# Kernel optimization log

Hardware: AMD Instinct MI355X
Metric: run time of the kernel (lower is better)

The kernel has to match this reference:

```python
import jax, jax.numpy as jnp
import numpy as np

B, S, E, H = 8, 1024, 1024, 16
D = E // H            # head_dim = 64
L = 1024              # pos_max_len; rpe table rows = 2*L+1
SCALE = D ** 0.5


def setup_inputs() -> dict:
    key = jax.random.key(0)
    ks = jax.random.split(key, 7)
    x = jax.random.normal(ks[0], (B, S, E), dtype=jnp.float32)
    mask = jnp.tril(jnp.ones((S, S), dtype=bool))[None, None]  # causal [1,1,S,S]
    w = 1.0 / np.sqrt(E)
    Wq = jax.random.normal(ks[1], (E, E), dtype=jnp.float32) * w
    Wk = jax.random.normal(ks[2], (E, E), dtype=jnp.float32) * w
    Wv = jax.random.normal(ks[3], (E, E), dtype=jnp.float32) * w
    Wo = jax.random.normal(ks[4], (E, E), dtype=jnp.float32) * w
    pek_table = jax.random.normal(ks[5], (2 * L + 1, D), dtype=jnp.float32) / D ** 0.5
    pev_table = jax.random.normal(ks[6], (2 * L + 1, D), dtype=jnp.float32) / D ** 0.5
    return {"x": x, "mask": mask, "Wq": Wq, "Wk": Wk, "Wv": Wv, "Wo": Wo,
            "pek_table": pek_table, "pev_table": pev_table}


def reference(x, mask, Wq, Wk, Wv, Wo, pek_table, pev_table):
    # QKV projections (torch Linear: y = x @ W.T), reshaped to [B,H,S,D]
    q = (x @ Wq.T).reshape(B, S, H, D).transpose(0, 2, 1, 3)
    k = (x @ Wk.T).reshape(B, S, H, D).transpose(0, 2, 1, 3)
    v = (x @ Wv.T).reshape(B, S, H, D).transpose(0, 2, 1, 3)

    scores = jnp.einsum('bhsd,bhtd->bhst', q, k) / SCALE  # [B,H,S,S]

    # relative-position embeddings: rel[i,j] selects embedding for offset j-i
    pos = jnp.arange(S)
    rel = jnp.clip(pos[None, :] - pos[:, None] + L, 0, 2 * L)  # [S,S]
    pek = pek_table[rel]  # [S,S,D]
    pev = pev_table[rel]  # [S,S,D]

    # RPE score term, replicating torch view/transpose semantics exactly:
    # Q2: [B,S,H,D] -> [S,B,H,D] -> [S, B*H, D]
    q2 = (x @ Wq.T).reshape(B, S, H, D).transpose(1, 0, 2, 3).reshape(S, B * H, D)
    s2 = jnp.einsum('snd,std->snt', q2, pek)               # [S, B*H, S]
    s2 = s2.reshape(S, H, B, S).transpose(2, 1, 0, 3)      # torch .view(S,H,B,S).transpose(0,2)
    scores = scores + s2 / SCALE

    scores = jnp.where(mask, scores, -jnp.inf)
    attn = jax.nn.softmax(scores, axis=-1)                  # [B,H,S,S]

    out = jnp.einsum('bhst,bhtd->bhsd', attn, v)            # [B,H,S,D]

    # RPE value term: attn.transpose(0,2) -> [S,H,B,S] -> [S, H*B, S]
    a2 = attn.transpose(2, 1, 0, 3).reshape(S, H * B, S)
    o2 = jnp.einsum('snt,std->snd', a2, pev)                # [S, H*B, D]
    o2 = o2.reshape(S, H, B, D).transpose(2, 1, 0, 3)       # [B,H,S,D]
    out = out + o2

    out = out.transpose(0, 2, 1, 3).reshape(B, S, E) @ Wo.T
    return out
```

## Files before the change

kernel.cpp:

```cpp
#include <hip/hip_runtime.h>
#include <math.h>

#define NB 8
#define NS 1024
#define NE 1024
#define NH 16
#define ND 64
#define NL 1024

typedef __attribute__((ext_vector_type(8))) short short8;
typedef __attribute__((ext_vector_type(4))) float f32x4;
typedef __attribute__((ext_vector_type(16))) float f32x16;

__device__ __forceinline__ ushort f2bf(float f) {
    union { __bf16 h; ushort u; } v;
    v.h = (__bf16)f;
    return v.u;
}
__device__ __forceinline__ float bf2f(ushort u) {
    union { unsigned u; float f; } v; v.u = ((unsigned)u) << 16;
    return v.f;
}

__device__ __forceinline__ void stage16(const ushort* gsrc, ushort* lbase) {
    __builtin_amdgcn_global_load_lds((const __attribute__((address_space(1))) void*)gsrc,
                                     (__attribute__((address_space(3))) void*)lbase,
                                     16, 0, 0);
}

__global__ __launch_bounds__(256)
void cast_f2b4(const float* __restrict__ in, ushort* __restrict__ out, int n4) {
    int i = blockIdx.x * 256 + threadIdx.x;
    if (i >= n4) return;
    float4 v = ((const float4*)in)[i];
    ((ushort4*)out)[i] = make_ushort4(f2bf(v.x), f2bf(v.y), f2bf(v.z), f2bf(v.w));
}

__global__ __launch_bounds__(256)
void cast_w4(const float* __restrict__ Wq, const float* __restrict__ Wk,
             const float* __restrict__ Wv, const float* __restrict__ Wo,
             ushort* __restrict__ out) {
    int i = blockIdx.x * 256 + threadIdx.x;
    const int seg = i >> 18, j = i & 262143;
    const float* src = seg == 0 ? Wq : seg == 1 ? Wk : seg == 2 ? Wv : Wo;
    float4 v = ((const float4*)src)[j];
    ((ushort4*)out)[i] = make_ushort4(f2bf(v.x), f2bf(v.y), f2bf(v.z), f2bf(v.w));
}

__global__ __launch_bounds__(256)
void cast_pek(const float* __restrict__ pek, ushort* __restrict__ out, int n) {
    int i = blockIdx.x * 256 + threadIdx.x;
    if (i >= n) return;
    const int r = i >> 6, d = i & 63;
    out[(size_t)(d >> 4) * 32784 + (size_t)r * 16 + (d & 15)] = f2bf(pek[i]);
}

__global__ __launch_bounds__(256)
void cast_pevt(const float* __restrict__ pev, ushort* __restrict__ out) {
    int i = blockIdx.x * 256 + threadIdx.x;
    if (i >= 64 * 1056) return;
    const int d = i / 1056, r = i % 1056;
    const int m = r >> 5, cc = (r >> 4) & 1, hi = (r >> 3) & 1, j = r & 7;
    const int a = d >> 5, sl = d & 31;
    out[(size_t)m * 2048 + cc * 1024 + a * 512 + (sl * 2 + hi) * 8 + j] =
        f2bf(pev[(size_t)(r + 1) * ND + d]);
}

template<int MODE>
__global__ __launch_bounds__(256)
void gemm_mfma(const ushort* __restrict__ A, const ushort* __restrict__ W,
               float* __restrict__ Cf, ushort* __restrict__ Cb)
{
    constexpr int K = 1024;
    __shared__ __align__(16) ushort As[128 * 32];
    __shared__ __align__(16) ushort Bs[128 * 32];
    const int tid = threadIdx.x;
    const int w   = tid >> 6;
    const int l   = tid & 63;
    const int m0  = blockIdx.x * 128;
    const int n0  = blockIdx.y * 128;
    const int wr  = w >> 1, wc = w & 1;

    const int srow = 16 * w + (l >> 2);
    const int scol = (l & 3) * 8;
    const ushort* aptr = A + (size_t)(m0 + srow) * K + scol;
    const ushort* bptr = W + (size_t)(n0 + srow) * K + scol;
    ushort* asl = &As[w * 512];
    ushort* bsl = &Bs[w * 512];

    const int fl = l & 15, fk = (l >> 4) * 8;

    f32x4 acc[4][4] = {};

    for (int k0 = 0; k0 < K; k0 += 32) {
        __syncthreads();
        stage16(aptr + k0,                    asl);
        stage16(aptr + k0 + (size_t)64 * K,   asl + 2048);
        stage16(bptr + k0,                    bsl);
        stage16(bptr + k0 + (size_t)64 * K,   bsl + 2048);
        __syncthreads();

        short8 af[4], bf[4];
        #pragma unroll
        for (int i = 0; i < 4; ++i)
            af[i] = *(const short8*)&As[(wr * 64 + i * 16 + fl) * 32 + fk];
        #pragma unroll
        for (int j = 0; j < 4; ++j)
            bf[j] = *(const short8*)&Bs[(wc * 64 + j * 16 + fl) * 32 + fk];
        #pragma unroll
        for (int i = 0; i < 4; ++i)
            #pragma unroll
            for (int j = 0; j < 4; ++j)
                acc[i][j] = __builtin_amdgcn_mfma_f32_16x16x32_bf16(af[i], bf[j], acc[i][j], 0, 0, 0);
    }

    #pragma unroll
    for (int i = 0; i < 4; ++i) {
        #pragma unroll
        for (int j = 0; j < 4; ++j) {
            #pragma unroll
            for (int q = 0; q < 4; ++q) {
                const int m = m0 + wr * 64 + i * 16 + (l >> 4) * 4 + q;
                const int n = n0 + wc * 64 + j * 16 + fl;
                const float vv = acc[i][j][q];
                if (MODE == 0) {
                    const int b = m >> 10, s = m & 1023, h = n >> 6, d = n & 63;
                    Cb[(((size_t)b * NH + h) * NS + s) * ND + d] = f2bf(vv);
                } else if (MODE == 4) {
                    const int bh = (m >> 10) * 16 + (n >> 6), t = m & 1023, d = n & 63;
                    Cb[((size_t)bh * 4 + (d >> 4)) * 16384 + (size_t)t * 16 + (d & 15)] = f2bf(vv);
                } else if (MODE == 3) {
                    const int h = m >> 6, d = m & 63, b = n >> 10, s = n & 1023;
                    const int bh = b * 16 + h;
                    const int it = s >> 5, trel = s & 31;
                    const int c = trel >> 4, hi = (trel >> 3) & 1, jj = trel & 7;
                    const int a = d >> 5, sl = d & 31;
                    Cb[(size_t)bh * 65536 + it * 2048 +
                       ((a * 2 + c) * 64 + sl * 2 + hi) * 8 + jj] = f2bf(vv);
                } else {
                    Cf[(size_t)m * NE + n] = vv;
                }
            }
        }
    }
}

__global__ __launch_bounds__(64, 2)
void attn_mfma(const ushort* __restrict__ Qb, const ushort* __restrict__ Kf_,
               const ushort* __restrict__ Vf_, const ushort* __restrict__ PEKf,
               const ushort* __restrict__ PEVf, ushort* __restrict__ AO)
{
    const int idx = blockIdx.x;
    const int st  = 31 - (idx >> 7);
    const int bh  = idx & 127;
    const int b   = bh >> 4, h = bh & 15;
    const int n2  = h * NB + b;
    const int b2  = n2 >> 4, h2 = n2 & 15;
    const int s0  = st * 32;

    const int lane = threadIdx.x;
    const int sl   = lane & 31;
    const int hi   = lane >> 5;

    __shared__ __align__(16) ushort Mb[2][32][67];
    __shared__ __align__(16) ushort Pb[2][32][72];

    for (int t = lane; t < 2 * 32 * 72 / 2; t += 64) ((int*)Pb)[t] = 0;

    const ushort* qptr  = Qb + (((size_t)bh * NS) + s0 + sl) * ND + hi * 8;
    const ushort* q2ptr = Qb + ((((size_t)b2 * NH + h2) * NS) + s0 + sl) * ND + hi * 8;
    short8 qf[4], q2f[4];
    #pragma unroll
    for (int c = 0; c < 4; ++c) {
        qf[c]  = *(const short8*)(qptr  + 16 * c);
        q2f[c] = *(const short8*)(q2ptr + 16 * c);
    }

    const ushort* kfb  = Kf_ + (size_t)bh * 65536 + sl * 16 + hi * 8;
    const ushort* vfb  = Vf_ + (size_t)bh * 65536 + (sl * 2 + hi) * 8;
    const ushort* efb  = PEKf + sl * 16 + hi * 8;
    const ushort* pevw = PEVf + (size_t)(31 - st) * 2048 + (sl * 2 + hi) * 8;
    const int RBASE = NL - 31 - s0;

    auto mchunk = [&](int c, int dual, const short8* ef) {
        f32x16 cm = {};
        #pragma unroll
        for (int c4 = 0; c4 < 4; ++c4)
            cm = __builtin_amdgcn_mfma_f32_32x32x16_bf16(q2f[c4], ef[c4], cm, 0, 0, 0);
        #pragma unroll
        for (int q = 0; q < 16; ++q) {
            const int srow = (q & 3) + 8 * (q >> 2) + 4 * hi;
            const ushort bb = f2bf(cm[q]);
            Mb[c & 1][srow][sl] = bb;
            if (dual) Mb[(c + 1) & 1][srow][32 + sl] = bb;
        }
    };

    f32x16 acc0 = {}, acc1 = {};
    float mrow = -1e30f, lrow = 0.f;
    short8 kf[4], va[2][2], eaA[2][2], eaB[2][2], efn[4];

    {
        short8 e0[4], e1[4];
        #pragma unroll
        for (int c4 = 0; c4 < 4; ++c4) {
            e0[c4] = *(const short8*)(efb + (size_t)c4 * 32784 + (size_t)RBASE * 16);
            e1[c4] = *(const short8*)(efb + (size_t)c4 * 32784 + (size_t)(RBASE + 32) * 16);
        }
        __builtin_amdgcn_s_setprio(1);
        mchunk(0, 0, e0);
        mchunk(1, 1, e1);
        __builtin_amdgcn_s_setprio(0);
    }
    #pragma unroll
    for (int c = 0; c < 4; ++c)
        kf[c] = *(const short8*)(kfb + c * 16384);
    #pragma unroll
    for (int c = 0; c < 2; ++c)
        #pragma unroll
        for (int a = 0; a < 2; ++a)
            va[c][a] = *(const short8*)(vfb + (a * 2 + c) * 512);
    if (st >= 1) {
        #pragma unroll
        for (int c4 = 0; c4 < 4; ++c4)
            efn[c4] = *(const short8*)(efb + (size_t)c4 * 32784 + (size_t)(RBASE + 64) * 16);
    }

    for (int i = 0; i <= st; ++i) {
        const int t0 = i * 32;
        const int p  = i & 1;

        #pragma unroll
        for (int cc = 0; cc < 2; ++cc)
            #pragma unroll
            for (int a = 0; a < 2; ++a)
                eaB[cc][a] = *(const short8*)(pevw + (size_t)i * 2048 + cc * 1024 + a * 512);

        f32x16 csw = {};
        __builtin_amdgcn_s_setprio(1);
        #pragma unroll
        for (int c = 0; c < 4; ++c)
            csw = __builtin_amdgcn_mfma_f32_32x32x16_bf16(kf[c], qf[c], csw, 0, 0, 0);
        __builtin_amdgcn_s_setprio(0);

        if (i < st) {
            #pragma unroll
            for (int c = 0; c < 4; ++c)
                kf[c] = *(const short8*)(kfb + c * 16384 + (size_t)(t0 + 32) * 16);
        }

        float sc[16];
        #pragma unroll
        for (int q = 0; q < 16; ++q) {
            const int trow = (q & 3) + 8 * (q >> 2) + 4 * hi;
            const int u = trow + 31 - sl;
            sc[q] = (csw[q] + bf2f(Mb[p][sl][u])) * 0.125f;
        }
        if (i == st) {
            #pragma unroll
            for (int q = 0; q < 16; ++q) {
                const int trow = (q & 3) + 8 * (q >> 2) + 4 * hi;
                if (t0 + trow > s0 + sl) sc[q] = -1e30f;
            }
        }
        float tm8[8], tm4[4];
        #pragma unroll
        for (int q = 0; q < 8; ++q) tm8[q] = fmaxf(sc[q], sc[q + 8]);
        #pragma unroll
        for (int q = 0; q < 4; ++q) tm4[q] = fmaxf(tm8[q], tm8[q + 4]);
        float tmax = fmaxf(fmaxf(tm4[0], tm4[1]), fmaxf(tm4[2], tm4[3]));

        if (i > 0) {
            __builtin_amdgcn_s_setprio(1);
            short8 pk0 = *(const short8*)&Pb[p ^ 1][sl][0 + 8 * hi];
            acc0 = __builtin_amdgcn_mfma_f32_32x32x16_bf16(eaA[0][0], pk0, acc0, 0, 0, 0);
            acc1 = __builtin_amdgcn_mfma_f32_32x32x16_bf16(eaA[0][1], pk0, acc1, 0, 0, 0);
            short8 pk1 = *(const short8*)&Pb[p ^ 1][sl][16 + 8 * hi];
            acc0 = __builtin_amdgcn_mfma_f32_32x32x16_bf16(eaA[1][0], pk1, acc0, 0, 0, 0);
            acc1 = __builtin_amdgcn_mfma_f32_32x32x16_bf16(eaA[1][1], pk1, acc1, 0, 0, 0);
            short8 pk2 = *(const short8*)&Pb[p ^ 1][sl][32 + 8 * hi];
            acc0 = __builtin_amdgcn_mfma_f32_32x32x16_bf16(eaB[0][0], pk2, acc0, 0, 0, 0);
            acc1 = __builtin_amdgcn_mfma_f32_32x32x16_bf16(eaB[0][1], pk2, acc1, 0, 0, 0);
            short8 pk3 = *(const short8*)&Pb[p ^ 1][sl][48 + 8 * hi];
            acc0 = __builtin_amdgcn_mfma_f32_32x32x16_bf16(eaB[1][0], pk3, acc0, 0, 0, 0);
            acc1 = __builtin_amdgcn_mfma_f32_32x32x16_bf16(eaB[1][1], pk3, acc1, 0, 0, 0);
            __builtin_amdgcn_s_setprio(0);
        }
        #pragma unroll
        for (int cc = 0; cc < 2; ++cc)
            #pragma unroll
            for (int a = 0; a < 2; ++a)
                eaA[cc][a] = eaB[cc][a];

        tmax = fmaxf(tmax, __shfl_xor(tmax, 32));
        if (!__all(tmax <= mrow + 8.f)) {
            const float mnew = fmaxf(mrow, tmax);
            const float r = __expf(mrow - mnew);
            lrow *= r;
            acc0 *= r; acc1 *= r;
            mrow = mnew;
        }
        float ps[16];
        #pragma unroll
        for (int q = 0; q < 16; ++q) ps[q] = __expf(sc[q] - mrow);
        float ls8[8], ls4[4];
        #pragma unroll
        for (int q = 0; q < 8; ++q) ls8[q] = ps[q] + ps[q + 8];
        #pragma unroll
        for (int q = 0; q < 4; ++q) ls4[q] = ls8[q] + ls8[q + 4];
        float lsum = (ls4[0] + ls4[1]) + (ls4[2] + ls4[3]);
        lsum += __shfl_xor(lsum, 32);
        lrow += lsum;

        #pragma unroll
        for (int q = 0; q < 16; ++q) {
            const int trow = (q & 3) + 8 * (q >> 2) + 4 * hi;
            Pb[p][sl][trow + 31 - sl] = f2bf(ps[q]);
        }

        if (i < st) {
            __builtin_amdgcn_s_setprio(1);
            mchunk(i + 2, 1, efn);
            __builtin_amdgcn_s_setprio(0);
            if (i + 1 < st) {
                #pragma unroll
                for (int c4 = 0; c4 < 4; ++c4)
                    efn[c4] = *(const short8*)(efb + (size_t)c4 * 32784 +
                                               (size_t)(RBASE + 32 * (i + 3)) * 16);
            }
        }

        float sh[16];
        #pragma unroll
        for (int q = 0; q < 16; ++q) sh[q] = __shfl_xor(ps[q], 32);
        __builtin_amdgcn_s_setprio(1);
        #pragma unroll
        for (int c = 0; c < 2; ++c) {
            short8 bfrag;
            #pragma unroll
            for (int j = 0; j < 8; ++j) {
                float pv;
                if (j < 4) pv = hi ? sh[8 * c + 4 + j] : ps[8 * c + j];
                else       pv = hi ? ps[8 * c + j]     : sh[8 * c + j - 4];
                bfrag[j] = (short)f2bf(pv);
            }
            acc0 = __builtin_amdgcn_mfma_f32_32x32x16_bf16(va[c][0], bfrag, acc0, 0, 0, 0);
            acc1 = __builtin_amdgcn_mfma_f32_32x32x16_bf16(va[c][1], bfrag, acc1, 0, 0, 0);
        }
        __builtin_amdgcn_s_setprio(0);

        if (i < st) {
            #pragma unroll
            for (int c = 0; c < 2; ++c)
                #pragma unroll
                for (int a = 0; a < 2; ++a)
                    va[c][a] = *(const short8*)(vfb + (size_t)(i + 1) * 2048 + (a * 2 + c) * 512);
        }
    }

    {
        short8 eaF[2][2];
        #pragma unroll
        for (int cc = 0; cc < 2; ++cc)
            #pragma unroll
            for (int a = 0; a < 2; ++a)
                eaF[cc][a] = *(const short8*)(pevw + (size_t)(st + 1) * 2048 + cc * 1024 + a * 512);
        __builtin_amdgcn_s_setprio(1);
        short8 pk0 = *(const short8*)&Pb[st & 1][sl][0 + 8 * hi];
        acc0 = __builtin_amdgcn_mfma_f32_32x32x16_bf16(eaA[0][0], pk0, acc0, 0, 0, 0);
        acc1 = __builtin_amdgcn_mfma_f32_32x32x16_bf16(eaA[0][1], pk0, acc1, 0, 0, 0);
        short8 pk1 = *(const short8*)&Pb[st & 1][sl][16 + 8 * hi];
        acc0 = __builtin_amdgcn_mfma_f32_32x32x16_bf16(eaA[1][0], pk1, acc0, 0, 0, 0);
        acc1 = __builtin_amdgcn_mfma_f32_32x32x16_bf16(eaA[1][1], pk1, acc1, 0, 0, 0);
        short8 pk2 = *(const short8*)&Pb[st & 1][sl][32 + 8 * hi];
        acc0 = __builtin_amdgcn_mfma_f32_32x32x16_bf16(eaF[0][0], pk2, acc0, 0, 0, 0);
        acc1 = __builtin_amdgcn_mfma_f32_32x32x16_bf16(eaF[0][1], pk2, acc1, 0, 0, 0);
        short8 pk3 = *(const short8*)&Pb[st & 1][sl][48 + 8 * hi];
        acc0 = __builtin_amdgcn_mfma_f32_32x32x16_bf16(eaF[1][0], pk3, acc0, 0, 0, 0);
        acc1 = __builtin_amdgcn_mfma_f32_32x32x16_bf16(eaF[1][1], pk3, acc1, 0, 0, 0);
        __builtin_amdgcn_s_setprio(0);
    }

    const float inv = 1.0f / lrow;
    ushort* orow = AO + ((size_t)b * NS + s0 + sl) * NE + h * ND;
    #pragma unroll
    for (int g = 0; g < 4; ++g) {
        ushort4 o0 = make_ushort4(f2bf(acc0[4*g+0]*inv), f2bf(acc0[4*g+1]*inv),
                                  f2bf(acc0[4*g+2]*inv), f2bf(acc0[4*g+3]*inv));
        ushort4 o1 = make_ushort4(f2bf(acc1[4*g+0]*inv), f2bf(acc1[4*g+1]*inv),
                                  f2bf(acc1[4*g+2]*inv), f2bf(acc1[4*g+3]*inv));
        *(ushort4*)&orow[8 * g + 4 * hi]      = o0;
        *(ushort4*)&orow[8 * g + 4 * hi + 32] = o1;
    }
}

extern "C" void kernel_launch(void* const* d_in, const int* in_sizes, int n_in,
                              void* d_out, int out_size, void* d_ws, size_t ws_size,
                              hipStream_t stream) {
    const float* x   = (const float*)d_in[0];
    const float* Wq  = (const float*)d_in[2];
    const float* Wk  = (const float*)d_in[3];
    const float* Wv  = (const float*)d_in[4];
    const float* Wo  = (const float*)d_in[5];
    const float* pek = (const float*)d_in[6];
    const float* pev = (const float*)d_in[7];

    ushort* ws16 = (ushort*)d_ws;
    size_t off = 0;
    ushort* xb    = ws16 + off; off += (size_t)8388608;
    ushort* Wqb   = ws16 + off; off += (size_t)1048576;
    ushort* Wkb   = ws16 + off; off += (size_t)1048576;
    ushort* Wvb   = ws16 + off; off += (size_t)1048576;
    ushort* Wob   = ws16 + off; off += (size_t)1048576;
    ushort* Qb    = ws16 + off; off += (size_t)8388608;
    ushort* Kfm   = ws16 + off; off += (size_t)8388608;
    ushort* Vfm   = ws16 + off; off += (size_t)8388608;
    ushort* PEKf  = ws16 + off; off += (size_t)131136;
    ushort* PEVf  = ws16 + off; off += (size_t)67584;
    ushort* aob   = ws16 + off; off += (size_t)8388608;
    float*  out   = (float*)d_out;

    dim3 blk(256);
    cast_f2b4<<<8192, blk, 0, stream>>>(x, xb, 2097152);
    cast_w4<<<4096, blk, 0, stream>>>(Wq, Wk, Wv, Wo, Wqb);
    cast_pek<<<(2049 * 64 + 255) / 256, blk, 0, stream>>>(pek, PEKf, 2049 * 64);
    cast_pevt<<<(64 * 1056 + 255) / 256, blk, 0, stream>>>(pev, PEVf);

    gemm_mfma<0><<<dim3(64, 8), blk, 0, stream>>>(xb, Wqb, nullptr, Qb);
    gemm_mfma<4><<<dim3(64, 8), blk, 0, stream>>>(xb, Wkb, nullptr, Kfm);
    gemm_mfma<3><<<dim3(8, 64), blk, 0, stream>>>(Wvb, xb, nullptr, Vfm);

    attn_mfma<<<dim3(4096), dim3(64), 0, stream>>>(Qb, Kfm, Vfm, PEKf, PEVf, aob);

    gemm_mfma<1><<<dim3(64, 8), blk, 0, stream>>>(aob, Wob, out, nullptr);
}
```

Baseline: 231.1 us.

## Process key tiles in pairs to widen RPE value and score chunks

Restructures the attention main loop to handle two 32-key tiles per iteration. The RPE-key product is computed three chunks ahead into a wider double-buffered LDS tile. The RPE-value product now runs one 96-column MFMA pass per pair instead of a 64-column pass per tile, cutting the redundant overlap work. A single-tile tail loop handles the remainder. The register-level prefetching of K, V and PE fragments across iterations is dropped in favour of loads inside each iteration, which trades latency hiding for fewer live registers and may expose more memory latency.

```diff
diff --git a/kernel.cpp b/kernel.cpp
--- a/kernel.cpp
+++ b/kernel.cpp
@@ -162,10 +162,14 @@
     const int sl   = lane & 31;
     const int hi   = lane >> 5;
 
-    __shared__ __align__(16) ushort Mb[2][32][67];
-    __shared__ __align__(16) ushort Pb[2][32][72];
-
-    for (int t = lane; t < 2 * 32 * 72 / 2; t += 64) ((int*)Pb)[t] = 0;
+    const int T      = st + 1;
+    const int Ppairs = (T - 1) >> 1;
+    const int i0     = 2 * Ppairs;
+
+    __shared__ __align__(16) ushort Mp[2][32][99];
+    __shared__ __align__(16) ushort Pb2[32][98];
+
+    for (int t = lane; t < 32 * 98 / 2; t += 64) ((int*)Pb2)[t] = 0;
 
     const ushort* qptr  = Qb + (((size_t)bh * NS) + s0 + sl) * ND + hi * 8;
     const ushort* q2ptr = Qb + ((((size_t)b2 * NH + h2) * NS) + s0 + sl) * ND + hi * 8;
@@ -182,116 +186,79 @@
     const ushort* pevw = PEVf + (size_t)(31 - st) * 2048 + (sl * 2 + hi) * 8;
     const int RBASE = NL - 31 - s0;
 
-    auto mchunk = [&](int c, int dual, const short8* ef) {
+    auto mpchunk = [&](int c, int dst, int cb) {
         f32x16 cm = {};
         #pragma unroll
-        for (int c4 = 0; c4 < 4; ++c4)
-            cm = __builtin_amdgcn_mfma_f32_32x32x16_bf16(q2f[c4], ef[c4], cm, 0, 0, 0);
+        for (int c4 = 0; c4 < 4; ++c4) {
+            short8 ef = *(const short8*)(efb + (size_t)c4 * 32784 +
+                                         (size_t)(RBASE + 32 * c) * 16);
+            cm = __builtin_amdgcn_mfma_f32_32x32x16_bf16(q2f[c4], ef, cm, 0, 0, 0);
+        }
         #pragma unroll
         for (int q = 0; q < 16; ++q) {
             const int srow = (q & 3) + 8 * (q >> 2) + 4 * hi;
-            const ushort bb = f2bf(cm[q]);
-            Mb[c & 1][srow][sl] = bb;
-            if (dual) Mb[(c + 1) & 1][srow][32 + sl] = bb;
+            Mp[dst][srow][cb + sl] = f2bf(cm[q]);
         }
     };
 
     f32x16 acc0 = {}, acc1 = {};
     float mrow = -1e30f, lrow = 0.f;
-    short8 kf[4], va[2][2], eaA[2][2], eaB[2][2], efn[4];
-
-    {
-        short8 e0[4], e1[4];
-        #pragma unroll
-        for (int c4 = 0; c4 < 4; ++c4) {
-            e0[c4] = *(const short8*)(efb + (size_t)c4 * 32784 + (size_t)RBASE * 16);
-            e1[c4] = *(const short8*)(efb + (size_t)c4 * 32784 + (size_t)(RBASE + 32) * 16);
-        }
+    short8 eaA[2][2];
+
+    __builtin_amdgcn_s_setprio(1);
+    mpchunk(0, 0, 0);
+    mpchunk(1, 0, 32);
+    mpchunk(2, 0, 64);
+    __builtin_amdgcn_s_setprio(0);
+    #pragma unroll
+    for (int cc = 0; cc < 2; ++cc)
+        #pragma unroll
+        for (int a = 0; a < 2; ++a)
+            eaA[cc][a] = *(const short8*)(pevw + cc * 1024 + a * 512);
+
+    for (int k = 0; k < Ppairs; ++k) {
+        const int src = k & 1, dst = src ^ 1;
+        const int t0  = 64 * k;
+
+        short8 kfA[4], kfB[4], vaA[2][2];
+        #pragma unroll
+        for (int c = 0; c < 4; ++c) {
+            kfA[c] = *(const short8*)(kfb + c * 16384 + (size_t)t0 * 16);
+            kfB[c] = *(const short8*)(kfb + c * 16384 + (size_t)(t0 + 32) * 16);
+        }
+        #pragma unroll
+        for (int c = 0; c < 2; ++c)
+            #pragma unroll
+            for (int a = 0; a < 2; ++a)
+                vaA[c][a] = *(const short8*)(vfb + (size_t)(2 * k) * 2048 + (a * 2 + c) * 512);
+
+        f32x16 csw0 = {}, csw1 = {};
         __builtin_amdgcn_s_setprio(1);
-        mchunk(0, 0, e0);
-        mchunk(1, 1, e1);
+        #pragma unroll
+        for (int c = 0; c < 4; ++c)
+            csw0 = __builtin_amdgcn_mfma_f32_32x32x16_bf16(kfA[c], qf[c], csw0, 0, 0, 0);
+        #pragma unroll
+        for (int c = 0; c < 4; ++c)
+            csw1 = __builtin_amdgcn_mfma_f32_32x32x16_bf16(kfB[c], qf[c], csw1, 0, 0, 0);
         __builtin_amdgcn_s_setprio(0);
-    }
-    #pragma unroll
-    for (int c = 0; c < 4; ++c)
-        kf[c] = *(const short8*)(kfb + c * 16384);
-    #pragma unroll
-    for (int c = 0; c < 2; ++c)
-        #pragma unroll
-        for (int a = 0; a < 2; ++a)
-            va[c][a] = *(const short8*)(vfb + (a * 2 + c) * 512);
-    if (st >= 1) {
-        #pragma unroll
-        for (int c4 = 0; c4 < 4; ++c4)
-            efn[c4] = *(const short8*)(efb + (size_t)c4 * 32784 + (size_t)(RBASE + 64) * 16);
-    }
-
-    for (int i = 0; i <= st; ++i) {
-        const int t0 = i * 32;
-        const int p  = i & 1;
-
-        #pragma unroll
-        for (int cc = 0; cc < 2; ++cc)
-            #pragma unroll
-            for (int a = 0; a < 2; ++a)
-                eaB[cc][a] = *(const short8*)(pevw + (size_t)i * 2048 + cc * 1024 + a * 512);
-
-        f32x16 csw = {};
-        __builtin_amdgcn_s_setprio(1);
-        #pragma unroll
-        for (int c = 0; c < 4; ++c)
-            csw = __builtin_amdgcn_mfma_f32_32x32x16_bf16(kf[c], qf[c], csw, 0, 0, 0);
-        __builtin_amdgcn_s_setprio(0);
-
-        if (i < st) {
-            #pragma unroll
-            for (int c = 0; c < 4; ++c)
-                kf[c] = *(const short8*)(kfb + c * 16384 + (size_t)(t0 + 32) * 16);
-        }
-
-        float sc[16];
+
+        float sc[32];
         #pragma unroll
         for (int q = 0; q < 16; ++q) {
             const int trow = (q & 3) + 8 * (q >> 2) + 4 * hi;
             const int u = trow + 31 - sl;
-            sc[q] = (csw[q] + bf2f(Mb[p][sl][u])) * 0.125f;
-        }
-        if (i == st) {
-            #pragma unroll
-            for (int q = 0; q < 16; ++q) {
-                const int trow = (q & 3) + 8 * (q >> 2) + 4 * hi;
-                if (t0 + trow > s0 + sl) sc[q] = -1e30f;
-            }
-        }
-        float tm8[8], tm4[4];
-        #pragma unroll
-        for (int q = 0; q < 8; ++q) tm8[q] = fmaxf(sc[q], sc[q + 8]);
+            sc[q]      = (csw0[q] + bf2f(Mp[src][sl][u]))      * 0.125f;
+            sc[16 + q] = (csw1[q] + bf2f(Mp[src][sl][u + 32])) * 0.125f;
+        }
+
+        float tm16[16], tm8[8], tm4[4];
+        #pragma unroll
+        for (int q = 0; q < 16; ++q) tm16[q] = fmaxf(sc[q], sc[q + 16]);
+        #pragma unroll
+        for (int q = 0; q < 8; ++q) tm8[q] = fmaxf(tm16[q], tm16[q + 8]);
         #pragma unroll
         for (int q = 0; q < 4; ++q) tm4[q] = fmaxf(tm8[q], tm8[q + 4]);
         float tmax = fmaxf(fmaxf(tm4[0], tm4[1]), fmaxf(tm4[2], tm4[3]));
-
-        if (i > 0) {
-            __builtin_amdgcn_s_setprio(1);
-            short8 pk0 = *(const short8*)&Pb[p ^ 1][sl][0 + 8 * hi];
-            acc0 = __builtin_amdgcn_mfma_f32_32x32x16_bf16(eaA[0][0], pk0, acc0, 0, 0, 0);
-            acc1 = __builtin_amdgcn_mfma_f32_32x32x16_bf16(eaA[0][1], pk0, acc1, 0, 0, 0);
-            short8 pk1 = *(const short8*)&Pb[p ^ 1][sl][16 + 8 * hi];
-            acc0 = __builtin_amdgcn_mfma_f32_32x32x16_bf16(eaA[1][0], pk1, acc0, 0, 0, 0);
-            acc1 = __builtin_amdgcn_mfma_f32_32x32x16_bf16(eaA[1][1], pk1, acc1, 0, 0, 0);
-            short8 pk2 = *(const short8*)&Pb[p ^ 1][sl][32 + 8 * hi];
-            acc0 = __builtin_amdgcn_mfma_f32_32x32x16_bf16(eaB[0][0], pk2, acc0, 0, 0, 0);
-            acc1 = __builtin_amdgcn_mfma_f32_32x32x16_bf16(eaB[0][1], pk2, acc1, 0, 0, 0);
-            short8 pk3 = *(const short8*)&Pb[p ^ 1][sl][48 + 8 * hi];
-            acc0 = __builtin_amdgcn_mfma_f32_32x32x16_bf16(eaB[1][0], pk3, acc0, 0, 0, 0);
-            acc1 = __builtin_amdgcn_mfma_f32_32x32x16_bf16(eaB[1][1], pk3, acc1, 0, 0, 0);
-            __builtin_amdgcn_s_setprio(0);
-        }
-        #pragma unroll
-        for (int cc = 0; cc < 2; ++cc)
-            #pragma unroll
-            for (int a = 0; a < 2; ++a)
-                eaA[cc][a] = eaB[cc][a];
-
         tmax = fmaxf(tmax, __shfl_xor(tmax, 32));
         if (!__all(tmax <= mrow + 8.f)) {
             const float mnew = fmaxf(mrow, tmax);
@@ -300,12 +267,14 @@
             acc0 *= r; acc1 *= r;
             mrow = mnew;
         }
-        float ps[16];
-        #pragma unroll
-        for (int q = 0; q < 16; ++q) ps[q] = __expf(sc[q] - mrow);
-        float ls8[8], ls4[4];
-        #pragma unroll
-        for (int q = 0; q < 8; ++q) ls8[q] = ps[q] + ps[q + 8];
+        float ps[32];
+        #pragma unroll
+        for (int q = 0; q < 32; ++q) ps[q] = __expf(sc[q] - mrow);
+        float ls16[16], ls8[8], ls4[4];
+        #pragma unroll
+        for (int q = 0; q < 16; ++q) ls16[q] = ps[q] + ps[q + 16];
+        #pragma unroll
+        for (int q = 0; q < 8; ++q) ls8[q] = ls16[q] + ls16[q + 8];
         #pragma unroll
         for (int q = 0; q < 4; ++q) ls4[q] = ls8[q] + ls8[q + 4];
         float lsum = (ls4[0] + ls4[1]) + (ls4[2] + ls4[3]);
@@ -315,70 +284,212 @@
         #pragma unroll
         for (int q = 0; q < 16; ++q) {
             const int trow = (q & 3) + 8 * (q >> 2) + 4 * hi;
-            Pb[p][sl][trow + 31 - sl] = f2bf(ps[q]);
-        }
-
-        if (i < st) {
-            __builtin_amdgcn_s_setprio(1);
-            mchunk(i + 2, 1, efn);
-            __builtin_amdgcn_s_setprio(0);
-            if (i + 1 < st) {
-                #pragma unroll
-                for (int c4 = 0; c4 < 4; ++c4)
-                    efn[c4] = *(const short8*)(efb + (size_t)c4 * 32784 +
-                                               (size_t)(RBASE + 32 * (i + 3)) * 16);
+            Pb2[sl][trow + 31 - sl]      = f2bf(ps[q]);
+            Pb2[sl][trow + 63 - sl]      = f2bf(ps[16 + q]);
+        }
+
+        __builtin_amdgcn_s_setprio(1);
+        mpchunk(2 * k + 2, dst, 0);
+        mpchunk(2 * k + 3, dst, 32);
+        mpchunk(2 * k + 4, dst, 64);
+        __builtin_amdgcn_s_setprio(0);
+
+        short8 eaB[2][2], eaC[2][2];
+        #pragma unroll
+        for (int cc = 0; cc < 2; ++cc)
+            #pragma unroll
+            for (int a = 0; a < 2; ++a) {
+                eaB[cc][a] = *(const short8*)(pevw + (size_t)(2 * k + 1) * 2048 + cc * 1024 + a * 512);
+                eaC[cc][a] = *(const short8*)(pevw + (size_t)(2 * k + 2) * 2048 + cc * 1024 + a * 512);
             }
-        }
-
-        float sh[16];
-        #pragma unroll
-        for (int q = 0; q < 16; ++q) sh[q] = __shfl_xor(ps[q], 32);
+
         __builtin_amdgcn_s_setprio(1);
         #pragma unroll
         for (int c = 0; c < 2; ++c) {
+            float shc[8];
+            #pragma unroll
+            for (int j = 0; j < 8; ++j) shc[j] = __shfl_xor(ps[8 * c + j], 32);
             short8 bfrag;
             #pragma unroll
             for (int j = 0; j < 8; ++j) {
                 float pv;
-                if (j < 4) pv = hi ? sh[8 * c + 4 + j] : ps[8 * c + j];
-                else       pv = hi ? ps[8 * c + j]     : sh[8 * c + j - 4];
+                if (j < 4) pv = hi ? shc[4 + j]    : ps[8 * c + j];
+                else       pv = hi ? ps[8 * c + j] : shc[j - 4];
+                bfrag[j] = (short)f2bf(pv);
+            }
+            acc0 = __builtin_amdgcn_mfma_f32_32x32x16_bf16(vaA[c][0], bfrag, acc0, 0, 0, 0);
+            acc1 = __builtin_amdgcn_mfma_f32_32x32x16_bf16(vaA[c][1], bfrag, acc1, 0, 0, 0);
+        }
+        short8 vaB[2][2];
+        #pragma unroll
+        for (int c = 0; c < 2; ++c)
+            #pragma unroll
+            for (int a = 0; a < 2; ++a)
+                vaB[c][a] = *(const short8*)(vfb + (size_t)(2 * k + 1) * 2048 + (a * 2 + c) * 512);
+        #pragma unroll
+        for (int c = 0; c < 2; ++c) {
+            float shc[8];
+            #pragma unroll
+            for (int j = 0; j < 8; ++j) shc[j] = __shfl_xor(ps[16 + 8 * c + j], 32);
+            short8 bfrag;
+            #pragma unroll
+            for (int j = 0; j < 8; ++j) {
+                float pv;
+                if (j < 4) pv = hi ? shc[4 + j]         : ps[16 + 8 * c + j];
+                else       pv = hi ? ps[16 + 8 * c + j] : shc[j - 4];
+                bfrag[j] = (short)f2bf(pv);
+            }
+            acc0 = __builtin_amdgcn_mfma_f32_32x32x16_bf16(vaB[c][0], bfrag, acc0, 0, 0, 0);
+            acc1 = __builtin_amdgcn_mfma_f32_32x32x16_bf16(vaB[c][1], bfrag, acc1, 0, 0, 0);
+        }
+
+        {
+            short8 pk0 = *(const short8*)&Pb2[sl][0 + 8 * hi];
+            acc0 = __builtin_amdgcn_mfma_f32_32x32x16_bf16(eaA[0][0], pk0, acc0, 0, 0, 0);
+            acc1 = __builtin_amdgcn_mfma_f32_32x32x16_bf16(eaA[0][1], pk0, acc1, 0, 0, 0);
+            short8 pk1 = *(const short8*)&Pb2[sl][16 + 8 * hi];
+            acc0 = __builtin_amdgcn_mfma_f32_32x32x16_bf16(eaA[1][0], pk1, acc0, 0, 0, 0);
+            acc1 = __builtin_amdgcn_mfma_f32_32x32x16_bf16(eaA[1][1], pk1, acc1, 0, 0, 0);
+            short8 pk2 = *(const short8*)&Pb2[sl][32 + 8 * hi];
+            acc0 = __builtin_amdgcn_mfma_f32_32x32x16_bf16(eaB[0][0], pk2, acc0, 0, 0, 0);
+            acc1 = __builtin_amdgcn_mfma_f32_32x32x16_bf16(eaB[0][1], pk2, acc1, 0, 0, 0);
+            short8 pk3 = *(const short8*)&Pb2[sl][48 + 8 * hi];
+            acc0 = __builtin_amdgcn_mfma_f32_32x32x16_bf16(eaB[1][0], pk3, acc0, 0, 0, 0);
+            acc1 = __builtin_amdgcn_mfma_f32_32x32x16_bf16(eaB[1][1], pk3, acc1, 0, 0, 0);
+            short8 pk4 = *(const short8*)&Pb2[sl][64 + 8 * hi];
+            acc0 = __builtin_amdgcn_mfma_f32_32x32x16_bf16(eaC[0][0], pk4, acc0, 0, 0, 0);
+            acc1 = __builtin_amdgcn_mfma_f32_32x32x16_bf16(eaC[0][1], pk4, acc1, 0, 0, 0);
+            short8 pk5 = *(const short8*)&Pb2[sl][80 + 8 * hi];
+            acc0 = __builtin_amdgcn_mfma_f32_32x32x16_bf16(eaC[1][0], pk5, acc0, 0, 0, 0);
+            acc1 = __builtin_amdgcn_mfma_f32_32x32x16_bf16(eaC[1][1], pk5, acc1, 0, 0, 0);
+        }
+        __builtin_amdgcn_s_setprio(0);
+
+        #pragma unroll
+        for (int cc = 0; cc < 2; ++cc)
+            #pragma unroll
+            for (int a = 0; a < 2; ++a)
+                eaA[cc][a] = eaC[cc][a];
+    }
+
+    for (int i = i0; i <= st; ++i) {
+        const int msrc = Ppairs & 1;
+        const int cb   = (i - i0) * 32;
+        const int t0   = i * 32;
+
+        short8 kf[4], va[2][2];
+        #pragma unroll
+        for (int c = 0; c < 4; ++c)
+            kf[c] = *(const short8*)(kfb + c * 16384 + (size_t)t0 * 16);
+        #pragma unroll
+        for (int c = 0; c < 2; ++c)
+            #pragma unroll
+            for (int a = 0; a < 2; ++a)
+                va[c][a] = *(const short8*)(vfb + (size_t)i * 2048 + (a * 2 + c) * 512);
+
+        f32x16 csw = {};
+        __builtin_amdgcn_s_setprio(1);
+        #pragma unroll
+        for (int c = 0; c < 4; ++c)
+            csw = __builtin_amdgcn_mfma_f32_32x32x16_bf16(kf[c], qf[c], csw, 0, 0, 0);
+        __builtin_amdgcn_s_setprio(0);
+
+        float sc[16];
+        #pragma unroll
+        for (int q = 0; q < 16; ++q) {
+            const int trow = (q & 3) + 8 * (q >> 2) + 4 * hi;
+            const int u = cb + trow + 31 - sl;
+            sc[q] = (csw[q] + bf2f(Mp[msrc][sl][u])) * 0.125f;
+        }
+        if (i == st) {
+            #pragma unroll
+            for (int q = 0; q < 16; ++q) {
+                const int trow = (q & 3) + 8 * (q >> 2) + 4 * hi;
+                if (t0 + trow > s0 + sl) sc[q] = -1e30f;
+            }
+        }
+        float tm8[8], tm4[4];
+        #pragma unroll
+        for (int q = 0; q < 8; ++q) tm8[q] = fmaxf(sc[q], sc[q + 8]);
+        #pragma unroll
+        for (int q = 0; q < 4; ++q) tm4[q] = fmaxf(tm8[q], tm8[q + 4]);
+        float tmax = fmaxf(fmaxf(tm4[0], tm4[1]), fmaxf(tm4[2], tm4[3]));
+        tmax = fmaxf(tmax, __shfl_xor(tmax, 32));
+        if (!__all(tmax <= mrow + 8.f)) {
+            const float mnew = fmaxf(mrow, tmax);
+            const float r = __expf(mrow - mnew);
+            lrow *= r;
+            acc0 *= r; acc1 *= r;
+            mrow = mnew;
+        }
+        float ps[16];
+        #pragma unroll
+        for (int q = 0; q < 16; ++q) ps[q] = __expf(sc[q] - mrow);
+        float ls8[8], ls4[4];
+        #pragma unroll
+        for (int q = 0; q < 8; ++q) ls8[q] = ps[q] + ps[q + 8];
+        #pragma unroll
+        for (int q = 0; q < 4; ++q) ls4[q] = ls8[q] + ls8[q + 4];
+        float lsum = (ls4[0] + ls4[1]) + (ls4[2] + ls4[3]);
+        lsum += __shfl_xor(lsum, 32);
+        lrow += lsum;
+
+        #pragma unroll
+        for (int q = 0; q < 16; ++q) {
+            const int trow = (q & 3) + 8 * (q >> 2) + 4 * hi;
+            Pb2[sl][trow + 31 - sl] = f2bf(ps[q]);
+        }
+        if (i == i0 && Ppairs > 0) {
+            #pragma unroll
+            for (int jj = 0; jj < 16; ++jj)
+                Pb2[sl][63 - sl + 16 * hi + jj] = 0;
+        }
+
+        __builtin_amdgcn_s_setprio(1);
+        #pragma unroll
+        for (int c = 0; c < 2; ++c) {
+            float shc[8];
+            #pragma unroll
+            for (int j = 0; j < 8; ++j) shc[j] = __shfl_xor(ps[8 * c + j], 32);
+            short8 bfrag;
+            #pragma unroll
+            for (int j = 0; j < 8; ++j) {
+                float pv;
+                if (j < 4) pv = hi ? shc[4 + j]    : ps[8 * c + j];
+                else       pv = hi ? ps[8 * c + j] : shc[j - 4];
                 bfrag[j] = (short)f2bf(pv);
             }
             acc0 = __builtin_amdgcn_mfma_f32_32x32x16_bf16(va[c][0], bfrag, acc0, 0, 0, 0);
             acc1 = __builtin_amdgcn_mfma_f32_32x32x16_bf16(va[c][1], bfrag, acc1, 0, 0, 0);
         }
+
+        short8 eaF[2][2];
+        #pragma unroll
+        for (int cc = 0; cc < 2; ++cc)
+            #pragma unroll
+            for (int a = 0; a < 2; ++a)
+                eaF[cc][a] = *(const short8*)(pevw + (size_t)(i + 1) * 2048 + cc * 1024 + a * 512);
+        {
+            short8 pk0 = *(const short8*)&Pb2[sl][0 + 8 * hi];
+            acc0 = __builtin_amdgcn_mfma_f32_32x32x16_bf16(eaA[0][0], pk0, acc0, 0, 0, 0);
+            acc1 = __builtin_amdgcn_mfma_f32_32x32x16_bf16(eaA[0][1], pk0, acc1, 0, 0, 0);
+            short8 pk1 = *(const short8*)&Pb2[sl][16 + 8 * hi];
+            acc0 = __builtin_amdgcn_mfma_f32_32x32x16_bf16(eaA[1][0], pk1, acc0, 0, 0, 0);
+            acc1 = __builtin_amdgcn_mfma_f32_32x32x16_bf16(eaA[1][1], pk1, acc1, 0, 0, 0);
+            short8 pk2 = *(const short8*)&Pb2[sl][32 + 8 * hi];
+            acc0 = __builtin_amdgcn_mfma_f32_32x32x16_bf16(eaF[0][0], pk2, acc0, 0, 0, 0);
+            acc1 = __builtin_amdgcn_mfma_f32_32x32x16_bf16(eaF[0][1], pk2, acc1, 0, 0, 0);
+            short8 pk3 = *(const short8*)&Pb2[sl][48 + 8 * hi];
+            acc0 = __builtin_amdgcn_mfma_f32_32x32x16_bf16(eaF[1][0], pk3, acc0, 0, 0, 0);
+            acc1 = __builtin_amdgcn_mfma_f32_32x32x16_bf16(eaF[1][1], pk3, acc1, 0, 0, 0);
+        }
         __builtin_amdgcn_s_setprio(0);
 
-        if (i < st) {
-            #pragma unroll
-            for (int c = 0; c < 2; ++c)
-                #pragma unroll
-                for (int a = 0; a < 2; ++a)
-                    va[c][a] = *(const short8*)(vfb + (size_t)(i + 1) * 2048 + (a * 2 + c) * 512);
-        }
-    }
-
-    {
-        short8 eaF[2][2];
         #pragma unroll
         for (int cc = 0; cc < 2; ++cc)
             #pragma unroll
             for (int a = 0; a < 2; ++a)
-                eaF[cc][a] = *(const short8*)(pevw + (size_t)(st + 1) * 2048 + cc * 1024 + a * 512);
-        __builtin_amdgcn_s_setprio(1);
-        short8 pk0 = *(const short8*)&Pb[st & 1][sl][0 + 8 * hi];
-        acc0 = __builtin_amdgcn_mfma_f32_32x32x16_bf16(eaA[0][0], pk0, acc0, 0, 0, 0);
-        acc1 = __builtin_amdgcn_mfma_f32_32x32x16_bf16(eaA[0][1], pk0, acc1, 0, 0, 0);
-        short8 pk1 = *(const short8*)&Pb[st & 1][sl][16 + 8 * hi];
-        acc0 = __builtin_amdgcn_mfma_f32_32x32x16_bf16(eaA[1][0], pk1, acc0, 0, 0, 0);
-        acc1 = __builtin_amdgcn_mfma_f32_32x32x16_bf16(eaA[1][1], pk1, acc1, 0, 0, 0);
-        short8 pk2 = *(const short8*)&Pb[st & 1][sl][32 + 8 * hi];
-        acc0 = __builtin_amdgcn_mfma_f32_32x32x16_bf16(eaF[0][0], pk2, acc0, 0, 0, 0);
-        acc1 = __builtin_amdgcn_mfma_f32_32x32x16_bf16(eaF[0][1], pk2, acc1, 0, 0, 0);
-        short8 pk3 = *(const short8*)&Pb[st & 1][sl][48 + 8 * hi];
-        acc0 = __builtin_amdgcn_mfma_f32_32x32x16_bf16(eaF[1][0], pk3, acc0, 0, 0, 0);
-        acc1 = __builtin_amdgcn_mfma_f32_32x32x16_bf16(eaF[1][1], pk3, acc1, 0, 0, 0);
-        __builtin_amdgcn_s_setprio(0);
+                eaA[cc][a] = eaF[cc][a];
     }
 
     const float inv = 1.0f / lrow;
```

Result: no change. 229.7 us (-0.6%).
